# Kernel optimization log

Hardware: AMD Instinct MI355X
Metric: run time of the kernel (lower is better)

The kernel has to match this reference:

```python
import jax, jax.numpy as jnp
from jax import lax
import numpy as np

B, C, H, W = 8, 256, 64, 64
STRIDE, NH = 2, 8
ED_QK, ED_V = 64, 256  # embed_dim//ratio (divisible by heads), embed_dim
HQ, WQ = H // STRIDE, W // STRIDE
L = HQ * WQ


def conv2d(x, w, b, stride=1, pad=0):
    y = lax.conv_general_dilated(x, w, (stride, stride), ((pad, pad), (pad, pad)),
                                 dimension_numbers=('NCHW', 'OIHW', 'NCHW'))
    return y + b[None, :, None, None]


def setup_inputs() -> dict:
    key = jax.random.key(0)
    ks = jax.random.split(key, 24)
    s = 0.05
    f32 = jnp.float32
    inp = {
        'qkv_pos': jax.random.normal(ks[0], (B, C, H, W), f32),
        'qkv_cha': jax.random.normal(ks[1], (B, C, H, W), f32),
        # POS branch params (standard convs)
        'Wq_pos': jax.random.normal(ks[2], (ED_QK, C, 2, 2), f32) * s,
        'bq_pos': jax.random.normal(ks[3], (ED_QK,), f32) * s,
        'Wk_pos': jax.random.normal(ks[4], (ED_QK, C, 2, 2), f32) * s,
        'bk_pos': jax.random.normal(ks[5], (ED_QK,), f32) * s,
        'Wv_pos': jax.random.normal(ks[6], (ED_V, C, 2, 2), f32) * s,
        'bv_pos': jax.random.normal(ks[7], (ED_V,), f32) * s,
        'Wo_pos': jax.random.normal(ks[8], (C, ED_V, 3, 3), f32) * s,
        'bo_pos': jax.random.normal(ks[9], (C,), f32) * s,
        'gamma_pos': jnp.full((1,), 0.5, f32),
        # CHA branch params (grouped convs, groups=C, 1 in-ch -> NH out-ch per group)
        'Wq_cha': jax.random.normal(ks[10], (C, NH, 2, 2), f32) * s,
        'bq_cha': jax.random.normal(ks[11], (C, NH), f32) * s,
        'Wk_cha': jax.random.normal(ks[12], (C, NH, 2, 2), f32) * s,
        'bk_cha': jax.random.normal(ks[13], (C, NH), f32) * s,
        'Wv_cha': jax.random.normal(ks[14], (C, NH, 2, 2), f32) * s,
        'bv_cha': jax.random.normal(ks[15], (C, NH), f32) * s,
        # grouped ConvTranspose2d (groups=C, NH in-ch per group -> 1 out-ch), k=s=2
        'Wt_cha': jax.random.normal(ks[16], (C, NH, 2, 2), f32) * s,
        'bt_cha': jax.random.normal(ks[17], (C,), f32) * s,
        'gamma_cha': jnp.full((1,), 0.5, f32),
        # fusion conv: concat -> 2C in, C out, 3x3
        'Wf': jax.random.normal(ks[18], (C, 2 * C, 3, 3), f32) * s,
        'bf': jax.random.normal(ks[19], (C,), f32) * s,
    }
    return inp


def _gproj(x, w, b):
    # grouped conv with kernel==stride==2, 1 in-ch per group -> NH out-ch per group
    xp = x.reshape(B, C, HQ, STRIDE, WQ, STRIDE)
    y = jnp.einsum('bgikjl,ghkl->bghij', xp, w) + b[None, :, :, None, None]
    # channel order c = g*NH + h (torch grouped-conv layout); torch then reshapes
    # the flat C*NH channels into (NH, C) -> same as a direct reshape here
    return y.reshape(B, NH, C, L)


def reference(qkv_pos, qkv_cha, Wq_pos, bq_pos, Wk_pos, bk_pos, Wv_pos, bv_pos,
              Wo_pos, bo_pos, gamma_pos, Wq_cha, bq_cha, Wk_cha, bk_cha,
              Wv_cha, bv_cha, Wt_cha, bt_cha, gamma_cha, Wf, bf):
    hd = ED_QK // NH
    # ---- POS (spatial) attention ----
    qp = conv2d(qkv_pos, Wq_pos, bq_pos, STRIDE).reshape(B, NH, hd, L).transpose(0, 1, 3, 2)
    kp = conv2d(qkv_pos, Wk_pos, bk_pos, STRIDE).reshape(B, NH, hd, L).transpose(0, 1, 3, 2)
    vp = conv2d(qkv_pos, Wv_pos, bv_pos, STRIDE).reshape(B, NH, ED_V // NH, L).transpose(0, 1, 3, 2)
    attn_p = jax.nn.softmax(jnp.einsum('bhqd,bhkd->bhqk', qp, kp) * (hd ** -0.5), axis=-1)
    op = jnp.einsum('bhqk,bhkd->bhqd', attn_p, vp).transpose(0, 1, 3, 2).reshape(B, ED_V, HQ, WQ)
    op = conv2d(op, Wo_pos, bo_pos, 1, 1)
    op = jax.image.resize(op, (B, C, H, W), 'bilinear')  # Upsample(align_corners=False)
    out_pos = qkv_pos + op * gamma_pos
    # ---- CHA (channel) attention ----
    qc = _gproj(qkv_cha, Wq_cha, bq_cha)  # [B,NH,C,L]
    kc = _gproj(qkv_cha, Wk_cha, bk_cha)
    vc = _gproj(qkv_cha, Wv_cha, bv_cha)
    attn_c = jax.nn.softmax(jnp.einsum('bhcl,bhdl->bhcd', qc, kc) * (L ** -0.5), axis=-1)
    oc = jnp.einsum('bhcd,bhdl->bhcl', attn_c, vc)  # [B,NH,C,L]
    # flat channel c = h*C + g; grouped ConvTranspose2d groups by c//NH -> reshape (C,NH)
    ocg = oc.reshape(B, C, NH, HQ, WQ)
    oc = jnp.einsum('bgipq,gikl->bgpkql', ocg, Wt_cha).reshape(B, C, H, W) + bt_cha[None, :, None, None]
    out_cha = qkv_cha + oc * gamma_cha
    # ---- fusion: concat (slices are full since slides=0) + 3x3 conv ----
    out = jnp.concatenate([out_pos, out_cha], axis=1)
    return conv2d(out, Wf, bf, 1, 1)
```

## Files before the change

kernel.cpp:

```cpp
#include <hip/hip_runtime.h>
#include <math.h>


typedef __attribute__((ext_vector_type(8))) short bf16x8;
typedef __attribute__((ext_vector_type(4))) float f32x4;

__device__ __forceinline__ ushort f2bf(float f) {
  union { float f; unsigned u; } v; v.f = f;
  unsigned r = (v.u + 0x7FFFu + ((v.u >> 16) & 1u)) >> 16;
  return (ushort)r;
}

template <int CIN>
__global__ __launch_bounds__(256) void k_prepack9(
    const float* __restrict__ W, ushort* __restrict__ out)
{
  const int i = blockIdx.x * 256 + threadIdx.x;
  const int t = i / (256 * CIN);
  const int r = i - t * (256 * CIN);
  const int oc = r / CIN;
  const int c = r - oc * CIN;
  out[i] = f2bf(W[((size_t)oc * CIN + c) * 9 + t]);
}

__global__ __launch_bounds__(256) void k_cast_wqkv(
    const float* __restrict__ Wq, const float* __restrict__ Wk,
    const float* __restrict__ Wv, ushort* __restrict__ out)
{
  const int i = blockIdx.x * 256 + threadIdx.x;
  const int o = i >> 10, k = i & 1023;
  float v;
  if (o < 64)       v = Wq[(size_t)o * 1024 + k];
  else if (o < 128) v = Wk[(size_t)(o - 64) * 1024 + k];
  else              v = Wv[(size_t)(o - 128) * 1024 + k];
  out[i] = f2bf(v);
}

__global__ __launch_bounds__(256) void k_pack_pos(
    const float* __restrict__ x, ushort* __restrict__ Ap)
{
  const int t = blockIdx.x * 256 + threadIdx.x;
  const int j4 = t & 7;
  const int i  = (t >> 3) & 31;
  const int c  = (t >> 8) & 255;
  const int b  = t >> 16;
  const float* xb = x + (((size_t)b * 256 + c) << 12) + (2 * i) * 64 + 8 * j4;
  union { float4 v[2]; float f[8]; } r0, r1;
  r0.v[0] = *(const float4*)(xb);
  r0.v[1] = *(const float4*)(xb + 4);
  r1.v[0] = *(const float4*)(xb + 64);
  r1.v[1] = *(const float4*)(xb + 68);
  #pragma unroll
  for (int jj = 0; jj < 4; ++jj) {
    const int l = i * 32 + j4 * 4 + jj;
    union { ushort u[4]; uint2 d; } pk;
    pk.u[0] = f2bf(r0.f[2 * jj]);
    pk.u[1] = f2bf(r0.f[2 * jj + 1]);
    pk.u[2] = f2bf(r1.f[2 * jj]);
    pk.u[3] = f2bf(r1.f[2 * jj + 1]);
    *(uint2*)(Ap + ((((size_t)b << 10) + l) << 10) + c * 4) = pk.d;
  }
}

__global__ __launch_bounds__(256) void k_pos_qkv_mfma(
    const ushort* __restrict__ Ap, const ushort* __restrict__ Wqkv,
    const float* __restrict__ bq, const float* __restrict__ bk,
    const float* __restrict__ bv,
    ushort* __restrict__ Qb, ushort* __restrict__ Kb, ushort* __restrict__ Vtb)
{
  const int n0 = blockIdx.x * 128, oc0 = blockIdx.y * 128, b = blockIdx.z;
  const int tid = threadIdx.x, lane = tid & 63, w = tid >> 6;
  __shared__ ushort As[128][32], Bs[128][32];
  const ushort* Abw = Wqkv + (size_t)oc0 * 1024;
  const ushort* Bb  = Ap + (((size_t)b << 10) + n0) * 1024;
  const int wr = w >> 1, wc = w & 1;
  f32x4 acc[4][4];
  #pragma unroll
  for (int mi = 0; mi < 4; ++mi)
    #pragma unroll
    for (int ni = 0; ni < 4; ++ni) {
      f32x4 z = {0.f, 0.f, 0.f, 0.f};
      acc[mi][ni] = z;
    }
  for (int kc = 0; kc < 1024; kc += 32) {
    __syncthreads();
    #pragma unroll
    for (int q = 0; q < 2; ++q) {
      int idx = w * 128 + q * 64 + lane;
      int row = idx >> 2, seg = idx & 3;
      const ushort* srcA = Abw + (size_t)row * 1024 + kc + seg * 8;
      const ushort* srcB = Bb + (size_t)row * 1024 + kc + seg * 8;
      char* dstA = (char*)&As[0][0] + w * 2048 + q * 1024;
      char* dstB = (char*)&Bs[0][0] + w * 2048 + q * 1024;
      __builtin_amdgcn_global_load_lds(
          (const __attribute__((address_space(1))) unsigned*)srcA,
          (__attribute__((address_space(3))) unsigned*)dstA, 16, 0, 0);
      __builtin_amdgcn_global_load_lds(
          (const __attribute__((address_space(1))) unsigned*)srcB,
          (__attribute__((address_space(3))) unsigned*)dstB, 16, 0, 0);
    }
    __syncthreads();
    bf16x8 af[4], bfv[4];
    #pragma unroll
    for (int mi = 0; mi < 4; ++mi)
      af[mi] = *(const bf16x8*)&As[wr * 64 + mi * 16 + (lane & 15)][(lane >> 4) * 8];
    #pragma unroll
    for (int ni = 0; ni < 4; ++ni)
      bfv[ni] = *(const bf16x8*)&Bs[wc * 64 + ni * 16 + (lane & 15)][(lane >> 4) * 8];
    #pragma unroll
    for (int mi = 0; mi < 4; ++mi)
      #pragma unroll
      for (int ni = 0; ni < 4; ++ni)
        acc[mi][ni] = __builtin_amdgcn_mfma_f32_16x16x32_bf16(
            af[mi], bfv[ni], acc[mi][ni], 0, 0, 0);
  }
  #pragma unroll
  for (int mi = 0; mi < 4; ++mi) {
    const int oc = oc0 + wr * 64 + mi * 16 + (lane >> 4) * 4;
    if (oc >= 384) continue;
    if (oc < 64) {
      const int hh = oc >> 3, e = oc & 7;
      float4 bb = *(const float4*)(bq + oc);
      #pragma unroll
      for (int ni = 0; ni < 4; ++ni) {
        const int l = n0 + wc * 64 + ni * 16 + (lane & 15);
        union { ushort u[4]; uint2 d; } pk;
        pk.u[0] = f2bf((acc[mi][ni][0] + bb.x) * 0.35355339059327373f);
        pk.u[1] = f2bf((acc[mi][ni][1] + bb.y) * 0.35355339059327373f);
        pk.u[2] = f2bf((acc[mi][ni][2] + bb.z) * 0.35355339059327373f);
        pk.u[3] = f2bf((acc[mi][ni][3] + bb.w) * 0.35355339059327373f);
        *(uint2*)(Qb + (((((size_t)b * 8 + hh) << 10) + l) << 5) + e) = pk.d;
      }
    } else if (oc < 128) {
      const int o2 = oc - 64, hh = o2 >> 3, e = o2 & 7;
      float4 bb = *(const float4*)(bk + o2);
      #pragma unroll
      for (int ni = 0; ni < 4; ++ni) {
        const int l = n0 + wc * 64 + ni * 16 + (lane & 15);
        union { ushort u[4]; uint2 d; } pk;
        pk.u[0] = f2bf(acc[mi][ni][0] + bb.x);
        pk.u[1] = f2bf(acc[mi][ni][1] + bb.y);
        pk.u[2] = f2bf(acc[mi][ni][2] + bb.z);
        pk.u[3] = f2bf(acc[mi][ni][3] + bb.w);
        *(uint2*)(Kb + (((((size_t)b * 8 + hh) << 10) + l) << 5) + e) = pk.d;
      }
    } else {
      const int o2 = oc - 128, hh = o2 >> 5, dd = o2 & 31;
      float4 bb = *(const float4*)(bv + o2);
      #pragma unroll
      for (int ni = 0; ni < 4; ++ni) {
        const int l = n0 + wc * 64 + ni * 16 + (lane & 15);
        ushort* vb = Vtb + ((((size_t)b * 8 + hh) * 32 + dd) << 10) + l;
        vb[0]      = f2bf(acc[mi][ni][0] + bb.x);
        vb[1024]   = f2bf(acc[mi][ni][1] + bb.y);
        vb[2048]   = f2bf(acc[mi][ni][2] + bb.z);
        vb[3072]   = f2bf(acc[mi][ni][3] + bb.w);
      }
    }
  }
}

__global__ __launch_bounds__(256) void k_pos_flash(
    const ushort* __restrict__ Qb, const ushort* __restrict__ Kb,
    const ushort* __restrict__ Vtb, ushort* __restrict__ op_pad)
{
  const int qt = blockIdx.x, h = blockIdx.y, b = blockIdx.z;
  const int bh = b * 8 + h;
  const int tid = threadIdx.x, lane = tid & 63, wq = tid >> 6;
  const int c = lane & 15, g = lane >> 4;
  __shared__ __align__(16) ushort Ps[4][32][72];
  const int qbase = qt * 128 + wq * 32;
  bf16x8 qf[2];
  #pragma unroll
  for (int nt = 0; nt < 2; ++nt)
    qf[nt] = *(const bf16x8*)(Qb + (((size_t)bh << 10) + qbase + nt * 16 + c) * 32 + g * 8);
  f32x4 o[2][2];
  #pragma unroll
  for (int mt = 0; mt < 2; ++mt)
    #pragma unroll
    for (int nt = 0; nt < 2; ++nt) {
      f32x4 z = {0.f, 0.f, 0.f, 0.f};
      o[mt][nt] = z;
    }
  float m[2] = {-1e30f, -1e30f}, l[2] = {0.f, 0.f};
  const ushort* Kbh = Kb + ((size_t)bh << 15);
  const ushort* Vbh = Vtb + ((size_t)bh << 15);

  for (int kt = 0; kt < 16; ++kt) {
    const int kb0 = kt * 64;
    bf16x8 kf[4];
    #pragma unroll
    for (int mt = 0; mt < 4; ++mt)
      kf[mt] = *(const bf16x8*)(Kbh + (size_t)(kb0 + mt * 16 + c) * 32 + g * 8);
    f32x4 s[4][2];
    #pragma unroll
    for (int mt = 0; mt < 4; ++mt)
      #pragma unroll
      for (int nt = 0; nt < 2; ++nt) {
        f32x4 z = {0.f, 0.f, 0.f, 0.f};
        s[mt][nt] = __builtin_amdgcn_mfma_f32_16x16x32_bf16(kf[mt], qf[nt], z, 0, 0, 0);
      }
    #pragma unroll
    for (int nt = 0; nt < 2; ++nt) {
      float tmax = -1e30f;
      #pragma unroll
      for (int mt = 0; mt < 4; ++mt)
        #pragma unroll
        for (int r = 0; r < 4; ++r)
          tmax = fmaxf(tmax, s[mt][nt][r]);
      tmax = fmaxf(tmax, __shfl_xor(tmax, 16, 64));
      tmax = fmaxf(tmax, __shfl_xor(tmax, 32, 64));
      const float mn = fmaxf(m[nt], tmax);
      const float alpha = __expf(m[nt] - mn);
      m[nt] = mn;
      float rs = 0.f;
      #pragma unroll
      for (int mt = 0; mt < 4; ++mt) {
        union { ushort u[4]; uint2 d; } pk;
        #pragma unroll
        for (int r = 0; r < 4; ++r) {
          float p = __expf(s[mt][nt][r] - mn);
          rs += p;
          pk.u[r] = f2bf(p);
        }
        *(uint2*)&Ps[wq][nt * 16 + c][mt * 16 + g * 4] = pk.d;
      }
      rs += __shfl_xor(rs, 16, 64);
      rs += __shfl_xor(rs, 32, 64);
      l[nt] = l[nt] * alpha + rs;
      #pragma unroll
      for (int mt = 0; mt < 2; ++mt)
        #pragma unroll
        for (int r = 0; r < 4; ++r)
          o[mt][nt][r] *= alpha;
    }
    #pragma unroll
    for (int kc = 0; kc < 2; ++kc) {
      bf16x8 vf[2], pf[2];
      #pragma unroll
      for (int mt = 0; mt < 2; ++mt)
        vf[mt] = *(const bf16x8*)(Vbh + (size_t)(mt * 16 + c) * 1024 + kb0 + kc * 32 + g * 8);
      #pragma unroll
      for (int nt = 0; nt < 2; ++nt)
        pf[nt] = *(const bf16x8*)&Ps[wq][nt * 16 + c][kc * 32 + g * 8];
      #pragma unroll
      for (int mt = 0; mt < 2; ++mt)
        #pragma unroll
        for (int nt = 0; nt < 2; ++nt)
          o[mt][nt] = __builtin_amdgcn_mfma_f32_16x16x32_bf16(vf[mt], pf[nt], o[mt][nt], 0, 0, 0);
    }
  }
  #pragma unroll
  for (int nt = 0; nt < 2; ++nt) {
    const float linv = 1.f / l[nt];
    const int q = qbase + nt * 16 + c;
    const int y = q >> 5, x = q & 31;
    ushort* dst = op_pad + ((size_t)b * 1156 + (y + 1) * 34 + (x + 1)) * 256 + h * 32;
    #pragma unroll
    for (int mt = 0; mt < 2; ++mt) {
      union { ushort u[4]; uint2 d; } pk;
      #pragma unroll
      for (int r = 0; r < 4; ++r)
        pk.u[r] = f2bf(o[mt][nt][r] * linv);
      *(uint2*)(dst + mt * 16 + g * 4) = pk.d;
    }
  }
}

template <int CIN, int S, int PW, int OUT_NHWC>
__global__ __launch_bounds__(256) void k_conv9_mfma(
    const ushort* __restrict__ in, const ushort* __restrict__ W9,
    const float* __restrict__ bias, float* __restrict__ out)
{
  const int n0 = blockIdx.x * 128, oc0 = blockIdx.y * 128, b = blockIdx.z;
  const int tid = threadIdx.x, lane = tid & 63, w = tid >> 6;
  __shared__ ushort As[128][32], Bs[128][32];
  const int wr = w >> 1, wc = w & 1;
  f32x4 acc[4][4];
  #pragma unroll
  for (int mi = 0; mi < 4; ++mi)
    #pragma unroll
    for (int ni = 0; ni < 4; ++ni) {
      f32x4 z = {0.f, 0.f, 0.f, 0.f};
      acc[mi][ni] = z;
    }
  int rowq[2], segq[2], basep[2];
  #pragma unroll
  for (int q = 0; q < 2; ++q) {
    int idx = w * 128 + q * 64 + lane;
    rowq[q] = idx >> 2;
    segq[q] = (idx & 3) * 8;
    int n = n0 + rowq[q];
    int y = n / S, x = n % S;
    basep[q] = y * PW + x;
  }
  const ushort* inb = in + (size_t)b * (PW * PW) * CIN;

  for (int t = 0; t < 9; ++t) {
    const int offp = (t / 3) * PW + (t % 3);
    const ushort* wt = W9 + (size_t)t * 256 * CIN;
    for (int kc = 0; kc < CIN; kc += 32) {
      __syncthreads();
      #pragma unroll
      for (int q = 0; q < 2; ++q) {
        const ushort* srcA = wt + (size_t)(oc0 + rowq[q]) * CIN + kc + segq[q];
        const ushort* srcB = inb + (size_t)(basep[q] + offp) * CIN + kc + segq[q];
        char* dstA = (char*)&As[0][0] + w * 2048 + q * 1024;
        char* dstB = (char*)&Bs[0][0] + w * 2048 + q * 1024;
        __builtin_amdgcn_global_load_lds(
            (const __attribute__((address_space(1))) unsigned*)srcA,
            (__attribute__((address_space(3))) unsigned*)dstA, 16, 0, 0);
        __builtin_amdgcn_global_load_lds(
            (const __attribute__((address_space(1))) unsigned*)srcB,
            (__attribute__((address_space(3))) unsigned*)dstB, 16, 0, 0);
      }
      __syncthreads();
      bf16x8 af[4], bfv[4];
      #pragma unroll
      for (int mi = 0; mi < 4; ++mi)
        af[mi] = *(const bf16x8*)&As[wr * 64 + mi * 16 + (lane & 15)][(lane >> 4) * 8];
      #pragma unroll
      for (int ni = 0; ni < 4; ++ni)
        bfv[ni] = *(const bf16x8*)&Bs[wc * 64 + ni * 16 + (lane & 15)][(lane >> 4) * 8];
      #pragma unroll
      for (int mi = 0; mi < 4; ++mi)
        #pragma unroll
        for (int ni = 0; ni < 4; ++ni)
          acc[mi][ni] = __builtin_amdgcn_mfma_f32_16x16x32_bf16(
              af[mi], bfv[ni], acc[mi][ni], 0, 0, 0);
    }
  }
  if (OUT_NHWC) {
    float* outb = out + (size_t)b * (S * S) * 256;
    #pragma unroll
    for (int mi = 0; mi < 4; ++mi) {
      const int oc = oc0 + wr * 64 + mi * 16 + (lane >> 4) * 4;
      float4 bb = *(const float4*)(bias + oc);
      #pragma unroll
      for (int ni = 0; ni < 4; ++ni) {
        const int n = n0 + wc * 64 + ni * 16 + (lane & 15);
        float4 v;
        v.x = acc[mi][ni][0] + bb.x;
        v.y = acc[mi][ni][1] + bb.y;
        v.z = acc[mi][ni][2] + bb.z;
        v.w = acc[mi][ni][3] + bb.w;
        *(float4*)(outb + (size_t)n * 256 + oc) = v;
      }
    }
  } else {
    float* outb = out + (size_t)b * 256 * (S * S);
    #pragma unroll
    for (int mi = 0; mi < 4; ++mi) {
      #pragma unroll
      for (int r = 0; r < 4; ++r) {
        int oc = oc0 + wr * 64 + mi * 16 + (lane >> 4) * 4 + r;
        float bb = bias[oc];
        #pragma unroll
        for (int ni = 0; ni < 4; ++ni) {
          int n = n0 + wc * 64 + ni * 16 + (lane & 15);
          outb[(size_t)oc * (S * S) + n] = acc[mi][ni][r] + bb;
        }
      }
    }
  }
}

__global__ __launch_bounds__(256) void k_upsample_nhwc(
    const float* __restrict__ xpos, const float* __restrict__ opc,
    const float* __restrict__ gamma, ushort* __restrict__ fused)
{
  const int t = blockIdx.x * 256 + threadIdx.x;
  const int c = (t & 63) * 4;
  const int pix = (t >> 6) & 4095;
  const int b = t >> 18;
  const int y = pix >> 6, xx = pix & 63;
  const int my = y >> 1;
  const int y0 = (y & 1) ? my : my - 1;
  const float fy = (y & 1) ? 0.25f : 0.75f;
  const int mx = xx >> 1;
  const int x0 = (xx & 1) ? mx : mx - 1;
  const float fx = (xx & 1) ? 0.25f : 0.75f;
  const int y0c = max(y0, 0), y1c = min(y0 + 1, 31);
  const int x0c = max(x0, 0), x1c = min(x0 + 1, 31);
  const float* base = opc + (size_t)b * 1024 * 256 + c;
  float4 v00 = *(const float4*)(base + (size_t)(y0c * 32 + x0c) * 256);
  float4 v01 = *(const float4*)(base + (size_t)(y0c * 32 + x1c) * 256);
  float4 v10 = *(const float4*)(base + (size_t)(y1c * 32 + x0c) * 256);
  float4 v11 = *(const float4*)(base + (size_t)(y1c * 32 + x1c) * 256);
  const float w00 = (1.f - fy) * (1.f - fx), w01 = (1.f - fy) * fx;
  const float w10 = fy * (1.f - fx), w11 = fy * fx;
  const float g = gamma[0];
  const float* xr = xpos + ((size_t)b * 256 + c) * 4096 + pix;
  union { ushort u[4]; uint2 q; } o;
  o.u[0] = f2bf(xr[0]          + g * (w00 * v00.x + w01 * v01.x + w10 * v10.x + w11 * v11.x));
  o.u[1] = f2bf(xr[4096]       + g * (w00 * v00.y + w01 * v01.y + w10 * v10.y + w11 * v11.y));
  o.u[2] = f2bf(xr[2 * 4096]   + g * (w00 * v00.z + w01 * v01.z + w10 * v10.z + w11 * v11.z));
  o.u[3] = f2bf(xr[3 * 4096]   + g * (w00 * v00.w + w01 * v01.w + w10 * v10.w + w11 * v11.w));
  *(uint2*)(fused + ((size_t)b * 4356 + (y + 1) * 66 + (xx + 1)) * 512 + c) = o.q;
}

__global__ __launch_bounds__(256) void k_cha_proj(
    const float* __restrict__ x,
    const float* __restrict__ Wq, const float* __restrict__ bq,
    const float* __restrict__ Wk, const float* __restrict__ bk,
    const float* __restrict__ Wv, const float* __restrict__ bv,
    ushort* __restrict__ Qc, ushort* __restrict__ Kc, ushort* __restrict__ Vt)
{
  const int t = blockIdx.x * 256 + threadIdx.x;
  const int bl = t >> 16;
  const int g  = (t >> 8) & 255;
  const int lq = t & 255;
  const int i = lq >> 3, j4 = (lq & 7) << 2;
  const float* xb = x + (((size_t)bl * 256 + g) << 12) + (2 * i) * 64 + 2 * j4;
  union { float4 v[2]; float f[8]; } xr0, xr1;
  xr0.v[0] = *(const float4*)(xb);
  xr0.v[1] = *(const float4*)(xb + 4);
  xr1.v[0] = *(const float4*)(xb + 64);
  xr1.v[1] = *(const float4*)(xb + 68);
  const int bhl = bl * 8 + (g >> 5);
  const int c2b = (g & 31) * 8;
  const int l0 = i * 32 + j4;
  #pragma unroll
  for (int h = 0; h < 8; ++h) {
    float4 w4 = *(const float4*)(Wq + g * 32 + h * 4);
    float bb = bq[g * 8 + h];
    union { ushort u[4]; uint2 q; } o;
    #pragma unroll
    for (int jj = 0; jj < 4; ++jj) {
      float v = xr0.f[2 * jj] * w4.x + xr0.f[2 * jj + 1] * w4.y
              + xr1.f[2 * jj] * w4.z + xr1.f[2 * jj + 1] * w4.w + bb;
      o.u[jj] = f2bf(v * 0.03125f);
    }
    *(uint2*)(Qc + (((size_t)bhl * 256 + c2b + h) << 10) + l0) = o.q;
  }
  #pragma unroll
  for (int h = 0; h < 8; ++h) {
    float4 w4 = *(const float4*)(Wk + g * 32 + h * 4);
    float bb = bk[g * 8 + h];
    union { ushort u[4]; uint2 q; } o;
    #pragma unroll
    for (int jj = 0; jj < 4; ++jj) {
      float v = xr0.f[2 * jj] * w4.x + xr0.f[2 * jj + 1] * w4.y
              + xr1.f[2 * jj] * w4.z + xr1.f[2 * jj + 1] * w4.w + bb;
      o.u[jj] = f2bf(v);
    }
    *(uint2*)(Kc + (((size_t)bhl * 256 + c2b + h) << 10) + l0) = o.q;
  }
  ushort vo[4][8];
  #pragma unroll
  for (int h = 0; h < 8; ++h) {
    float4 w4 = *(const float4*)(Wv + g * 32 + h * 4);
    float bb = bv[g * 8 + h];
    #pragma unroll
    for (int jj = 0; jj < 4; ++jj) {
      float v = xr0.f[2 * jj] * w4.x + xr0.f[2 * jj + 1] * w4.y
              + xr1.f[2 * jj] * w4.z + xr1.f[2 * jj + 1] * w4.w + bb;
      vo[jj][h] = f2bf(v);
    }
  }
  #pragma unroll
  for (int jj = 0; jj < 4; ++jj)
    *(uint4*)(Vt + ((size_t)bhl << 18) + (size_t)(l0 + jj) * 256 + c2b) =
        *(uint4*)&vo[jj][0];
}

__global__ __launch_bounds__(256) void k_cha_scores_mfma(
    const ushort* __restrict__ Qc, const ushort* __restrict__ Kc,
    float* __restrict__ S)
{
  const int c0 = blockIdx.x * 128, d0 = blockIdx.y * 128, bhl = blockIdx.z;
  const int tid = threadIdx.x, lane = tid & 63, w = tid >> 6;
  __shared__ ushort As[128][32], Bs[128][32];
  const ushort* Ab = Qc + ((size_t)bhl * 256 + c0) * 1024;
  const ushort* Bb = Kc + ((size_t)bhl * 256 + d0) * 1024;
  const int wr = w >> 1, wc = w & 1;
  f32x4 acc[4][4];
  #pragma unroll
  for (int mi = 0; mi < 4; ++mi)
    #pragma unroll
    for (int ni = 0; ni < 4; ++ni) {
      f32x4 z = {0.f, 0.f, 0.f, 0.f};
      acc[mi][ni] = z;
    }
  for (int kc = 0; kc < 1024; kc += 32) {
    __syncthreads();
    #pragma unroll
    for (int q = 0; q < 2; ++q) {
      int idx = w * 128 + q * 64 + lane;
      int row = idx >> 2, seg = idx & 3;
      const ushort* srcA = Ab + (size_t)row * 1024 + kc + seg * 8;
      const ushort* srcB = Bb + (size_t)row * 1024 + kc + seg * 8;
      char* dstA = (char*)&As[0][0] + w * 2048 + q * 1024;
      char* dstB = (char*)&Bs[0][0] + w * 2048 + q * 1024;
      __builtin_amdgcn_global_load_lds(
          (const __attribute__((address_space(1))) unsigned*)srcA,
          (__attribute__((address_space(3))) unsigned*)dstA, 16, 0, 0);
      __builtin_amdgcn_global_load_lds(
          (const __attribute__((address_space(1))) unsigned*)srcB,
          (__attribute__((address_space(3))) unsigned*)dstB, 16, 0, 0);
    }
    __syncthreads();
    bf16x8 af[4], bfv[4];
    #pragma unroll
    for (int mi = 0; mi < 4; ++mi)
      af[mi] = *(const bf16x8*)&As[wr * 64 + mi * 16 + (lane & 15)][(lane >> 4) * 8];
    #pragma unroll
    for (int ni = 0; ni < 4; ++ni)
      bfv[ni] = *(const bf16x8*)&Bs[wc * 64 + ni * 16 + (lane & 15)][(lane >> 4) * 8];
    #pragma unroll
    for (int mi = 0; mi < 4; ++mi)
      #pragma unroll
      for (int ni = 0; ni < 4; ++ni)
        acc[mi][ni] = __builtin_amdgcn_mfma_f32_16x16x32_bf16(
            af[mi], bfv[ni], acc[mi][ni], 0, 0, 0);
  }
  float* Sb = S + ((size_t)bhl << 16);
  #pragma unroll
  for (int mi = 0; mi < 4; ++mi)
    #pragma unroll
    for (int r = 0; r < 4; ++r) {
      int c = c0 + wr * 64 + mi * 16 + (lane >> 4) * 4 + r;
      #pragma unroll
      for (int ni = 0; ni < 4; ++ni) {
        int d = d0 + wc * 64 + ni * 16 + (lane & 15);
        Sb[(size_t)c * 256 + d] = acc[mi][ni][r];
      }
    }
}

__global__ __launch_bounds__(256) void k_softmax_p(
    const float* __restrict__ S, ushort* __restrict__ P)
{
  const int row = blockIdx.x * 4 + (threadIdx.x >> 6);
  const int lane = threadIdx.x & 63;
  const float* r = S + (size_t)row * 256;
  float4 v = *(const float4*)(r + lane * 4);
  float m = fmaxf(fmaxf(v.x, v.y), fmaxf(v.z, v.w));
  #pragma unroll
  for (int off = 32; off; off >>= 1) m = fmaxf(m, __shfl_xor(m, off, 64));
  v.x = __expf(v.x - m); v.y = __expf(v.y - m);
  v.z = __expf(v.z - m); v.w = __expf(v.w - m);
  float s = v.x + v.y + v.z + v.w;
  #pragma unroll
  for (int off = 32; off; off >>= 1) s += __shfl_xor(s, off, 64);
  const float inv = 1.f / s;
  union { ushort u[4]; uint2 q; } o;
  o.u[0] = f2bf(v.x * inv); o.u[1] = f2bf(v.y * inv);
  o.u[2] = f2bf(v.z * inv); o.u[3] = f2bf(v.w * inv);
  *(uint2*)(P + (size_t)row * 256 + lane * 4) = o.q;
}

__global__ __launch_bounds__(256) void k_cha_pv(
    const ushort* __restrict__ P, const ushort* __restrict__ Vt,
    const float* __restrict__ x,
    const float* __restrict__ Wt, const float* __restrict__ bt,
    const float* __restrict__ gamma, ushort* __restrict__ fused, int bbase)
{
  const int n0 = blockIdx.x * 128, c0 = blockIdx.y * 128, bhl = blockIdx.z;
  const int b = bbase + (bhl >> 3), h = bhl & 7;
  const int tid = threadIdx.x, lane = tid & 63, w = tid >> 6;
  __shared__ ushort As[128][32], Bs[128][32];
  __shared__ ushort Ot[512][16];
  __shared__ float wt_s[16][32];
  __shared__ float bt_s[16];
  const int gp_base = h * 32 + (c0 >> 3);
  {
    int e = tid;
    wt_s[e >> 5][e & 31] = Wt[(size_t)gp_base * 32 + e];
    e += 256;
    wt_s[e >> 5][e & 31] = Wt[(size_t)gp_base * 32 + e];
    if (tid < 16) bt_s[tid] = bt[gp_base + tid];
  }
  const ushort* Ab = P + (((size_t)bhl << 8) + c0) * 256;
  const ushort* Bb = Vt + ((size_t)bhl << 18) + (size_t)n0 * 256;
  const int wr = w >> 1, wc = w & 1;
  f32x4 acc[4][4];
  #pragma unroll
  for (int mi = 0; mi < 4; ++mi)
    #pragma unroll
    for (int ni = 0; ni < 4; ++ni) {
      f32x4 z = {0.f, 0.f, 0.f, 0.f};
      acc[mi][ni] = z;
    }
  for (int kc = 0; kc < 256; kc += 32) {
    __syncthreads();
    #pragma unroll
    for (int q = 0; q < 2; ++q) {
      int idx = w * 128 + q * 64 + lane;
      int row = idx >> 2, seg = idx & 3;
      const ushort* srcA = Ab + (size_t)row * 256 + kc + seg * 8;
      const ushort* srcB = Bb + (size_t)row * 256 + kc + seg * 8;
      char* dstA = (char*)&As[0][0] + w * 2048 + q * 1024;
      char* dstB = (char*)&Bs[0][0] + w * 2048 + q * 1024;
      __builtin_amdgcn_global_load_lds(
          (const __attribute__((address_space(1))) unsigned*)srcA,
          (__attribute__((address_space(3))) unsigned*)dstA, 16, 0, 0);
      __builtin_amdgcn_global_load_lds(
          (const __attribute__((address_space(1))) unsigned*)srcB,
          (__attribute__((address_space(3))) unsigned*)dstB, 16, 0, 0);
    }
    __syncthreads();
    bf16x8 af[4], bfv[4];
    #pragma unroll
    for (int mi = 0; mi < 4; ++mi)
      af[mi] = *(const bf16x8*)&As[wr * 64 + mi * 16 + (lane & 15)][(lane >> 4) * 8];
    #pragma unroll
    for (int ni = 0; ni < 4; ++ni)
      bfv[ni] = *(const bf16x8*)&Bs[wc * 64 + ni * 16 + (lane & 15)][(lane >> 4) * 8];
    #pragma unroll
    for (int mi = 0; mi < 4; ++mi)
      #pragma unroll
      for (int ni = 0; ni < 4; ++ni)
        acc[mi][ni] = __builtin_amdgcn_mfma_f32_16x16x32_bf16(
            af[mi], bfv[ni], acc[mi][ni], 0, 0, 0);
  }
  const float gm = gamma[0];
  const int col = lane & 15, q = lane >> 4;
  #pragma unroll
  for (int mi = 0; mi < 4; ++mi) {
    const int gloc = wr * 8 + mi * 2 + (q >> 1);
    const int gp = gp_base + gloc;
    const float btv = bt_s[gloc];
    #pragma unroll
    for (int ni = 0; ni < 4; ++ni) {
      float pa[4] = {0.f, 0.f, 0.f, 0.f};
      #pragma unroll
      for (int r = 0; r < 4; ++r) {
        const int i2 = (q & 1) * 4 + r;
        const float a = acc[mi][ni][r];
        pa[0] += a * wt_s[gloc][i2 * 4 + 0];
        pa[1] += a * wt_s[gloc][i2 * 4 + 1];
        pa[2] += a * wt_s[gloc][i2 * 4 + 2];
        pa[3] += a * wt_s[gloc][i2 * 4 + 3];
      }
      float v0 = pa[0] + __shfl_xor(pa[0], 16, 64);
      float v1 = pa[1] + __shfl_xor(pa[1], 16, 64);
      float v2 = pa[2] + __shfl_xor(pa[2], 16, 64);
      float v3 = pa[3] + __shfl_xor(pa[3], 16, 64);
      const int lloc = wc * 64 + ni * 16 + col;
      const int l = n0 + lloc;
      const int p = l >> 5, j = l & 31;
      const int y = 2 * p + (q & 1);
      const float va = (q & 1) ? v2 : v0;
      const float vb = (q & 1) ? v3 : v1;
      const float* xc = x + (((size_t)b * 256 + gp) << 12) + (y << 6) + 2 * j;
      const int lp = (lloc << 2) + (q & 1) * 2;
      Ot[lp][gloc]     = f2bf(xc[0] + gm * (va + btv));
      Ot[lp + 1][gloc] = f2bf(xc[1] + gm * (vb + btv));
    }
  }
  __syncthreads();
  #pragma unroll
  for (int pp2 = 0; pp2 < 2; ++pp2) {
    const int pixl = tid * 2 + pp2;
    const int lloc = pixl >> 2;
    const int l = n0 + lloc;
    const int p = l >> 5, j = l & 31;
    const int yy = 2 * p + ((pixl >> 1) & 1) + 1;
    const int xx = 2 * j + (pixl & 1) + 1;
    const uint4* src = (const uint4*)&Ot[pixl][0];
    uint4* dst = (uint4*)(fused + ((size_t)b * 4356 + yy * 66 + xx) * 512 + 256 + gp_base);
    dst[0] = src[0];
    dst[1] = src[1];
  }
}

extern "C" void kernel_launch(void* const* d_in, const int* in_sizes, int n_in,
                              void* d_out, int out_size, void* d_ws, size_t ws_size,
                              hipStream_t stream)
{
  (void)in_sizes; (void)n_in; (void)out_size; (void)ws_size;
  const float* qkv_pos   = (const float*)d_in[0];
  const float* qkv_cha   = (const float*)d_in[1];
  const float* Wq_pos    = (const float*)d_in[2];
  const float* bq_pos    = (const float*)d_in[3];
  const float* Wk_pos    = (const float*)d_in[4];
  const float* bk_pos    = (const float*)d_in[5];
  const float* Wv_pos    = (const float*)d_in[6];
  const float* bv_pos    = (const float*)d_in[7];
  const float* Wo_pos    = (const float*)d_in[8];
  const float* bo_pos    = (const float*)d_in[9];
  const float* gamma_pos = (const float*)d_in[10];
  const float* Wq_cha    = (const float*)d_in[11];
  const float* bq_cha    = (const float*)d_in[12];
  const float* Wk_cha    = (const float*)d_in[13];
  const float* bk_cha    = (const float*)d_in[14];
  const float* Wv_cha    = (const float*)d_in[15];
  const float* bv_cha    = (const float*)d_in[16];
  const float* Wt_cha    = (const float*)d_in[17];
  const float* bt_cha    = (const float*)d_in[18];
  const float* gamma_cha = (const float*)d_in[19];
  const float* Wf        = (const float*)d_in[20];
  const float* bf        = (const float*)d_in[21];
  float* out = (float*)d_out;

  float* ws = (float*)d_ws;
  ushort* Wpf9    = (ushort*)ws;
  ushort* Wpo9    = (ushort*)(ws + 589824);
  ushort* Qb      = (ushort*)(ws + 884736);
  ushort* Kb      = (ushort*)(ws + 1933312);
  ushort* Vtb     = (ushort*)(ws + 2981888);
  ushort* op_pad  = (ushort*)(ws + 4030464);
  float*  op_conv = ws + 5214208;
  ushort* Ap      = (ushort*)(ws + 7311360);
  ushort* qcb     = (ushort*)(ws + 884736);
  ushort* kcb     = (ushort*)(ws + 5079040);
  ushort* vcT     = (ushort*)(ws + 9273344);
  float*  attn_c  = ws + 13467648;
  ushort* Pb      = (ushort*)(ws + 15564800);
  ushort* fusedb  = (ushort*)(ws + 16613376);
  ushort* Wqkvp   = (ushort*)(ws + 25534464);

  hipMemsetAsync(op_pad, 0, (size_t)2367488 * 2, stream);
  hipMemsetAsync(fusedb, 0, (size_t)17842176 * 2, stream);
  hipMemsetAsync(Qb, 0, (size_t)2097152 * 2, stream);
  k_prepack9<512><<<dim3(4608), 256, 0, stream>>>(Wf, Wpf9);
  k_prepack9<256><<<dim3(2304), 256, 0, stream>>>(Wo_pos, Wpo9);
  k_cast_wqkv<<<dim3(1536), 256, 0, stream>>>(Wq_pos, Wk_pos, Wv_pos, Wqkvp);
  k_pack_pos<<<dim3(2048), 256, 0, stream>>>(qkv_pos, Ap);
  k_pos_qkv_mfma<<<dim3(8, 3, 8), 256, 0, stream>>>(Ap, Wqkvp,
      bq_pos, bk_pos, bv_pos, Qb, Kb, Vtb);
  k_pos_flash<<<dim3(8, 8, 8), 256, 0, stream>>>(Qb, Kb, Vtb, op_pad);
  k_conv9_mfma<256, 32, 34, 1><<<dim3(8, 2, 8), 256, 0, stream>>>(
      op_pad, Wpo9, bo_pos, op_conv);
  k_upsample_nhwc<<<dim3(8192), 256, 0, stream>>>(qkv_pos, op_conv, gamma_pos, fusedb);
  for (int half = 0; half < 2; ++half) {
    const float* xh = qkv_cha + (size_t)half * 4 * 256 * 4096;
    k_cha_proj<<<dim3(1024), 256, 0, stream>>>(xh, Wq_cha, bq_cha,
        Wk_cha, bk_cha, Wv_cha, bv_cha, qcb, kcb, vcT);
    k_cha_scores_mfma<<<dim3(2, 2, 32), 256, 0, stream>>>(qcb, kcb, attn_c);
    k_softmax_p<<<dim3(2048), 256, 0, stream>>>(attn_c, Pb);
    k_cha_pv<<<dim3(8, 2, 32), 256, 0, stream>>>(Pb, vcT, qkv_cha,
        Wt_cha, bt_cha, gamma_cha, fusedb, half * 4);
  }
  k_conv9_mfma<512, 64, 66, 0><<<dim3(32, 2, 8), 256, 0, stream>>>(
      fusedb, Wpf9, bf, out);
}
```

Baseline: 574.0 us.

## Double-buffer LDS tiles in MFMA GEMM kernels and flatten grid with batch-fastest order

Converts the four MFMA GEMM/conv kernels to double-buffered LDS, issuing the async global-to-LDS loads for the next K chunk before computing on the current one, with one barrier per iteration instead of two. This is meant to overlap memory latency with MFMA work. The conv kernels also merge the tap and channel loops into one flat chunk loop. Separately, the grids are flattened to 1D with batch as the fastest index, so concurrent blocks share weight tiles in cache. LDS use per block doubles, which may reduce occupancy.

```diff
diff --git a/kernel.cpp b/kernel.cpp
--- a/kernel.cpp
+++ b/kernel.cpp
@@ -10,6 +10,10 @@
   unsigned r = (v.u + 0x7FFFu + ((v.u >> 16) & 1u)) >> 16;
   return (ushort)r;
 }
+
+#define GLDS(src, dst) __builtin_amdgcn_global_load_lds( \
+    (const __attribute__((address_space(1))) unsigned*)(src), \
+    (__attribute__((address_space(3))) unsigned*)(dst), 16, 0, 0)
 
 template <int CIN>
 __global__ __launch_bounds__(256) void k_prepack9(
@@ -68,12 +72,16 @@
     const float* __restrict__ bv,
     ushort* __restrict__ Qb, ushort* __restrict__ Kb, ushort* __restrict__ Vtb)
 {
-  const int n0 = blockIdx.x * 128, oc0 = blockIdx.y * 128, b = blockIdx.z;
+  const int flat = blockIdx.x;
+  const int b = flat & 7;
+  const int t2 = flat >> 3;
+  const int n0 = (t2 & 7) * 128, oc0 = (t2 >> 3) * 128;
   const int tid = threadIdx.x, lane = tid & 63, w = tid >> 6;
-  __shared__ ushort As[128][32], Bs[128][32];
+  __shared__ ushort As[2][128][32], Bs[2][128][32];
   const ushort* Abw = Wqkv + (size_t)oc0 * 1024;
   const ushort* Bb  = Ap + (((size_t)b << 10) + n0) * 1024;
   const int wr = w >> 1, wc = w & 1;
+  const int rowq = (w * 128 + lane) >> 2 << 0;
   f32x4 acc[4][4];
   #pragma unroll
   for (int mi = 0; mi < 4; ++mi)
@@ -82,31 +90,34 @@
       f32x4 z = {0.f, 0.f, 0.f, 0.f};
       acc[mi][ni] = z;
     }
-  for (int kc = 0; kc < 1024; kc += 32) {
+  int rq[2], sq[2];
+  #pragma unroll
+  for (int q = 0; q < 2; ++q) {
+    int idx = w * 128 + q * 64 + lane;
+    rq[q] = idx >> 2;
+    sq[q] = (idx & 3) * 8;
+  }
+  auto issue = [&](int buf, int kc) {
+    #pragma unroll
+    for (int q = 0; q < 2; ++q) {
+      GLDS(Abw + (size_t)rq[q] * 1024 + kc + sq[q],
+           (char*)&As[buf][0][0] + w * 2048 + q * 1024);
+      GLDS(Bb + (size_t)rq[q] * 1024 + kc + sq[q],
+           (char*)&Bs[buf][0][0] + w * 2048 + q * 1024);
+    }
+  };
+  issue(0, 0);
+  for (int ck = 0; ck < 32; ++ck) {
+    const int buf = ck & 1;
     __syncthreads();
-    #pragma unroll
-    for (int q = 0; q < 2; ++q) {
-      int idx = w * 128 + q * 64 + lane;
-      int row = idx >> 2, seg = idx & 3;
-      const ushort* srcA = Abw + (size_t)row * 1024 + kc + seg * 8;
-      const ushort* srcB = Bb + (size_t)row * 1024 + kc + seg * 8;
-      char* dstA = (char*)&As[0][0] + w * 2048 + q * 1024;
-      char* dstB = (char*)&Bs[0][0] + w * 2048 + q * 1024;
-      __builtin_amdgcn_global_load_lds(
-          (const __attribute__((address_space(1))) unsigned*)srcA,
-          (__attribute__((address_space(3))) unsigned*)dstA, 16, 0, 0);
-      __builtin_amdgcn_global_load_lds(
-          (const __attribute__((address_space(1))) unsigned*)srcB,
-          (__attribute__((address_space(3))) unsigned*)dstB, 16, 0, 0);
-    }
-    __syncthreads();
+    if (ck + 1 < 32) issue(buf ^ 1, (ck + 1) * 32);
     bf16x8 af[4], bfv[4];
     #pragma unroll
     for (int mi = 0; mi < 4; ++mi)
-      af[mi] = *(const bf16x8*)&As[wr * 64 + mi * 16 + (lane & 15)][(lane >> 4) * 8];
+      af[mi] = *(const bf16x8*)&As[buf][wr * 64 + mi * 16 + (lane & 15)][(lane >> 4) * 8];
     #pragma unroll
     for (int ni = 0; ni < 4; ++ni)
-      bfv[ni] = *(const bf16x8*)&Bs[wc * 64 + ni * 16 + (lane & 15)][(lane >> 4) * 8];
+      bfv[ni] = *(const bf16x8*)&Bs[buf][wc * 64 + ni * 16 + (lane & 15)][(lane >> 4) * 8];
     #pragma unroll
     for (int mi = 0; mi < 4; ++mi)
       #pragma unroll
@@ -114,6 +125,7 @@
         acc[mi][ni] = __builtin_amdgcn_mfma_f32_16x16x32_bf16(
             af[mi], bfv[ni], acc[mi][ni], 0, 0, 0);
   }
+  (void)rowq;
   #pragma unroll
   for (int mi = 0; mi < 4; ++mi) {
     const int oc = oc0 + wr * 64 + mi * 16 + (lane >> 4) * 4;
@@ -272,9 +284,16 @@
     const ushort* __restrict__ in, const ushort* __restrict__ W9,
     const float* __restrict__ bias, float* __restrict__ out)
 {
-  const int n0 = blockIdx.x * 128, oc0 = blockIdx.y * 128, b = blockIdx.z;
+  constexpr int NT = (S * S) / 128;
+  constexpr int KCH = CIN / 32;
+  constexpr int NCH = 9 * KCH;
+  const int flat = blockIdx.x;
+  const int b = flat & 7;
+  const int t2 = flat >> 3;
+  const int n0 = (t2 % NT) * 128;
+  const int oc0 = (t2 / NT) * 128;
   const int tid = threadIdx.x, lane = tid & 63, w = tid >> 6;
-  __shared__ ushort As[128][32], Bs[128][32];
+  __shared__ ushort As[2][128][32], Bs[2][128][32];
   const int wr = w >> 1, wc = w & 1;
   f32x4 acc[4][4];
   #pragma unroll
@@ -284,51 +303,48 @@
       f32x4 z = {0.f, 0.f, 0.f, 0.f};
       acc[mi][ni] = z;
     }
-  int rowq[2], segq[2], basep[2];
+  int rq[2], sq[2], basep[2];
   #pragma unroll
   for (int q = 0; q < 2; ++q) {
     int idx = w * 128 + q * 64 + lane;
-    rowq[q] = idx >> 2;
-    segq[q] = (idx & 3) * 8;
-    int n = n0 + rowq[q];
+    rq[q] = idx >> 2;
+    sq[q] = (idx & 3) * 8;
+    int n = n0 + rq[q];
     int y = n / S, x = n % S;
     basep[q] = y * PW + x;
   }
   const ushort* inb = in + (size_t)b * (PW * PW) * CIN;
-
-  for (int t = 0; t < 9; ++t) {
+  auto issue = [&](int buf, int ck) {
+    const int t = ck / KCH;
+    const int kc = (ck - t * KCH) * 32;
     const int offp = (t / 3) * PW + (t % 3);
     const ushort* wt = W9 + (size_t)t * 256 * CIN;
-    for (int kc = 0; kc < CIN; kc += 32) {
-      __syncthreads();
-      #pragma unroll
-      for (int q = 0; q < 2; ++q) {
-        const ushort* srcA = wt + (size_t)(oc0 + rowq[q]) * CIN + kc + segq[q];
-        const ushort* srcB = inb + (size_t)(basep[q] + offp) * CIN + kc + segq[q];
-        char* dstA = (char*)&As[0][0] + w * 2048 + q * 1024;
-        char* dstB = (char*)&Bs[0][0] + w * 2048 + q * 1024;
-        __builtin_amdgcn_global_load_lds(
-            (const __attribute__((address_space(1))) unsigned*)srcA,
-            (__attribute__((address_space(3))) unsigned*)dstA, 16, 0, 0);
-        __builtin_amdgcn_global_load_lds(
-            (const __attribute__((address_space(1))) unsigned*)srcB,
-            (__attribute__((address_space(3))) unsigned*)dstB, 16, 0, 0);
-      }
-      __syncthreads();
-      bf16x8 af[4], bfv[4];
-      #pragma unroll
-      for (int mi = 0; mi < 4; ++mi)
-        af[mi] = *(const bf16x8*)&As[wr * 64 + mi * 16 + (lane & 15)][(lane >> 4) * 8];
+    #pragma unroll
+    for (int q = 0; q < 2; ++q) {
+      GLDS(wt + (size_t)(oc0 + rq[q]) * CIN + kc + sq[q],
+           (char*)&As[buf][0][0] + w * 2048 + q * 1024);
+      GLDS(inb + (size_t)(basep[q] + offp) * CIN + kc + sq[q],
+           (char*)&Bs[buf][0][0] + w * 2048 + q * 1024);
+    }
+  };
+  issue(0, 0);
+  for (int ck = 0; ck < NCH; ++ck) {
+    const int buf = ck & 1;
+    __syncthreads();
+    if (ck + 1 < NCH) issue(buf ^ 1, ck + 1);
+    bf16x8 af[4], bfv[4];
+    #pragma unroll
+    for (int mi = 0; mi < 4; ++mi)
+      af[mi] = *(const bf16x8*)&As[buf][wr * 64 + mi * 16 + (lane & 15)][(lane >> 4) * 8];
+    #pragma unroll
+    for (int ni = 0; ni < 4; ++ni)
+      bfv[ni] = *(const bf16x8*)&Bs[buf][wc * 64 + ni * 16 + (lane & 15)][(lane >> 4) * 8];
+    #pragma unroll
+    for (int mi = 0; mi < 4; ++mi)
       #pragma unroll
       for (int ni = 0; ni < 4; ++ni)
-        bfv[ni] = *(const bf16x8*)&Bs[wc * 64 + ni * 16 + (lane & 15)][(lane >> 4) * 8];
-      #pragma unroll
-      for (int mi = 0; mi < 4; ++mi)
-        #pragma unroll
-        for (int ni = 0; ni < 4; ++ni)
-          acc[mi][ni] = __builtin_amdgcn_mfma_f32_16x16x32_bf16(
-              af[mi], bfv[ni], acc[mi][ni], 0, 0, 0);
-    }
+        acc[mi][ni] = __builtin_amdgcn_mfma_f32_16x16x32_bf16(
+            af[mi], bfv[ni], acc[mi][ni], 0, 0, 0);
   }
   if (OUT_NHWC) {
     float* outb = out + (size_t)b * (S * S) * 256;
@@ -470,7 +486,7 @@
 {
   const int c0 = blockIdx.x * 128, d0 = blockIdx.y * 128, bhl = blockIdx.z;
   const int tid = threadIdx.x, lane = tid & 63, w = tid >> 6;
-  __shared__ ushort As[128][32], Bs[128][32];
+  __shared__ ushort As[2][128][32], Bs[2][128][32];
   const ushort* Ab = Qc + ((size_t)bhl * 256 + c0) * 1024;
   const ushort* Bb = Kc + ((size_t)bhl * 256 + d0) * 1024;
   const int wr = w >> 1, wc = w & 1;
@@ -482,31 +498,34 @@
       f32x4 z = {0.f, 0.f, 0.f, 0.f};
       acc[mi][ni] = z;
     }
-  for (int kc = 0; kc < 1024; kc += 32) {
+  int rq[2], sq[2];
+  #pragma unroll
+  for (int q = 0; q < 2; ++q) {
+    int idx = w * 128 + q * 64 + lane;
+    rq[q] = idx >> 2;
+    sq[q] = (idx & 3) * 8;
+  }
+  auto issue = [&](int buf, int kc) {
+    #pragma unroll
+    for (int q = 0; q < 2; ++q) {
+      GLDS(Ab + (size_t)rq[q] * 1024 + kc + sq[q],
+           (char*)&As[buf][0][0] + w * 2048 + q * 1024);
+      GLDS(Bb + (size_t)rq[q] * 1024 + kc + sq[q],
+           (char*)&Bs[buf][0][0] + w * 2048 + q * 1024);
+    }
+  };
+  issue(0, 0);
+  for (int ck = 0; ck < 32; ++ck) {
+    const int buf = ck & 1;
     __syncthreads();
-    #pragma unroll
-    for (int q = 0; q < 2; ++q) {
-      int idx = w * 128 + q * 64 + lane;
-      int row = idx >> 2, seg = idx & 3;
-      const ushort* srcA = Ab + (size_t)row * 1024 + kc + seg * 8;
-      const ushort* srcB = Bb + (size_t)row * 1024 + kc + seg * 8;
-      char* dstA = (char*)&As[0][0] + w * 2048 + q * 1024;
-      char* dstB = (char*)&Bs[0][0] + w * 2048 + q * 1024;
-      __builtin_amdgcn_global_load_lds(
-          (const __attribute__((address_space(1))) unsigned*)srcA,
-          (__attribute__((address_space(3))) unsigned*)dstA, 16, 0, 0);
-      __builtin_amdgcn_global_load_lds(
-          (const __attribute__((address_space(1))) unsigned*)srcB,
-          (__attribute__((address_space(3))) unsigned*)dstB, 16, 0, 0);
-    }
-    __syncthreads();
+    if (ck + 1 < 32) issue(buf ^ 1, (ck + 1) * 32);
     bf16x8 af[4], bfv[4];
     #pragma unroll
     for (int mi = 0; mi < 4; ++mi)
-      af[mi] = *(const bf16x8*)&As[wr * 64 + mi * 16 + (lane & 15)][(lane >> 4) * 8];
+      af[mi] = *(const bf16x8*)&As[buf][wr * 64 + mi * 16 + (lane & 15)][(lane >> 4) * 8];
     #pragma unroll
     for (int ni = 0; ni < 4; ++ni)
-      bfv[ni] = *(const bf16x8*)&Bs[wc * 64 + ni * 16 + (lane & 15)][(lane >> 4) * 8];
+      bfv[ni] = *(const bf16x8*)&Bs[buf][wc * 64 + ni * 16 + (lane & 15)][(lane >> 4) * 8];
     #pragma unroll
     for (int mi = 0; mi < 4; ++mi)
       #pragma unroll
@@ -559,7 +578,7 @@
   const int n0 = blockIdx.x * 128, c0 = blockIdx.y * 128, bhl = blockIdx.z;
   const int b = bbase + (bhl >> 3), h = bhl & 7;
   const int tid = threadIdx.x, lane = tid & 63, w = tid >> 6;
-  __shared__ ushort As[128][32], Bs[128][32];
+  __shared__ ushort As[2][128][32], Bs[2][128][32];
   __shared__ ushort Ot[512][16];
   __shared__ float wt_s[16][32];
   __shared__ float bt_s[16];
@@ -582,31 +601,34 @@
       f32x4 z = {0.f, 0.f, 0.f, 0.f};
       acc[mi][ni] = z;
     }
-  for (int kc = 0; kc < 256; kc += 32) {
+  int rq[2], sq[2];
+  #pragma unroll
+  for (int q = 0; q < 2; ++q) {
+    int idx = w * 128 + q * 64 + lane;
+    rq[q] = idx >> 2;
+    sq[q] = (idx & 3) * 8;
+  }
+  auto issue = [&](int buf, int kc) {
+    #pragma unroll
+    for (int q = 0; q < 2; ++q) {
+      GLDS(Ab + (size_t)rq[q] * 256 + kc + sq[q],
+           (char*)&As[buf][0][0] + w * 2048 + q * 1024);
+      GLDS(Bb + (size_t)rq[q] * 256 + kc + sq[q],
+           (char*)&Bs[buf][0][0] + w * 2048 + q * 1024);
+    }
+  };
+  issue(0, 0);
+  for (int ck = 0; ck < 8; ++ck) {
+    const int buf = ck & 1;
     __syncthreads();
-    #pragma unroll
-    for (int q = 0; q < 2; ++q) {
-      int idx = w * 128 + q * 64 + lane;
-      int row = idx >> 2, seg = idx & 3;
-      const ushort* srcA = Ab + (size_t)row * 256 + kc + seg * 8;
-      const ushort* srcB = Bb + (size_t)row * 256 + kc + seg * 8;
-      char* dstA = (char*)&As[0][0] + w * 2048 + q * 1024;
-      char* dstB = (char*)&Bs[0][0] + w * 2048 + q * 1024;
-      __builtin_amdgcn_global_load_lds(
-          (const __attribute__((address_space(1))) unsigned*)srcA,
-          (__attribute__((address_space(3))) unsigned*)dstA, 16, 0, 0);
-      __builtin_amdgcn_global_load_lds(
-          (const __attribute__((address_space(1))) unsigned*)srcB,
-          (__attribute__((address_space(3))) unsigned*)dstB, 16, 0, 0);
-    }
-    __syncthreads();
+    if (ck + 1 < 8) issue(buf ^ 1, (ck + 1) * 32);
     bf16x8 af[4], bfv[4];
     #pragma unroll
     for (int mi = 0; mi < 4; ++mi)
-      af[mi] = *(const bf16x8*)&As[wr * 64 + mi * 16 + (lane & 15)][(lane >> 4) * 8];
+      af[mi] = *(const bf16x8*)&As[buf][wr * 64 + mi * 16 + (lane & 15)][(lane >> 4) * 8];
     #pragma unroll
     for (int ni = 0; ni < 4; ++ni)
-      bfv[ni] = *(const bf16x8*)&Bs[wc * 64 + ni * 16 + (lane & 15)][(lane >> 4) * 8];
+      bfv[ni] = *(const bf16x8*)&Bs[buf][wc * 64 + ni * 16 + (lane & 15)][(lane >> 4) * 8];
     #pragma unroll
     for (int mi = 0; mi < 4; ++mi)
       #pragma unroll
@@ -718,10 +740,10 @@
   k_prepack9<256><<<dim3(2304), 256, 0, stream>>>(Wo_pos, Wpo9);
   k_cast_wqkv<<<dim3(1536), 256, 0, stream>>>(Wq_pos, Wk_pos, Wv_pos, Wqkvp);
   k_pack_pos<<<dim3(2048), 256, 0, stream>>>(qkv_pos, Ap);
-  k_pos_qkv_mfma<<<dim3(8, 3, 8), 256, 0, stream>>>(Ap, Wqkvp,
+  k_pos_qkv_mfma<<<dim3(192), 256, 0, stream>>>(Ap, Wqkvp,
       bq_pos, bk_pos, bv_pos, Qb, Kb, Vtb);
   k_pos_flash<<<dim3(8, 8, 8), 256, 0, stream>>>(Qb, Kb, Vtb, op_pad);
-  k_conv9_mfma<256, 32, 34, 1><<<dim3(8, 2, 8), 256, 0, stream>>>(
+  k_conv9_mfma<256, 32, 34, 1><<<dim3(128), 256, 0, stream>>>(
       op_pad, Wpo9, bo_pos, op_conv);
   k_upsample_nhwc<<<dim3(8192), 256, 0, stream>>>(qkv_pos, op_conv, gamma_pos, fusedb);
   for (int half = 0; half < 2; ++half) {
@@ -733,6 +755,6 @@
     k_cha_pv<<<dim3(8, 2, 32), 256, 0, stream>>>(Pb, vcT, qkv_cha,
         Wt_cha, bt_cha, gamma_cha, fusedb, half * 4);
   }
-  k_conv9_mfma<512, 64, 66, 0><<<dim3(32, 2, 8), 256, 0, stream>>>(
+  k_conv9_mfma<512, 64, 66, 0><<<dim3(512), 256, 0, stream>>>(
       fusedb, Wpf9, bf, out);
 }
```

After: 627.9 us. +9.4%, slower.
